# Kernel optimization log

Hardware: AMD Instinct MI355X
Metric: run time of the kernel (lower is better)

Reference implementation:

```python
import jax, jax.numpy as jnp
import numpy as np

DIM, E, H, HS = 2048, 8, 1408, 2816
B, S = 4, 2048


def setup_inputs() -> dict:
    key = jax.random.key(0)
    ks = jax.random.split(key, 12)
    sc = 0.02
    return {
        "x": jax.random.normal(ks[0], (B, S, DIM), jnp.float32),
        "gate_w": jax.random.normal(ks[1], (E, DIM), jnp.float32) * sc,
        "gate_b": jnp.zeros((E,), jnp.float32),
        "w1": jax.random.normal(ks[2], (E, H, DIM), jnp.float32) * sc,
        "b1": jnp.zeros((E, H), jnp.float32),
        "w3": jax.random.normal(ks[3], (E, H, DIM), jnp.float32) * sc,
        "b3": jnp.zeros((E, H), jnp.float32),
        "w2": jax.random.normal(ks[4], (E, DIM, H), jnp.float32) * sc,
        "b2": jnp.zeros((E, DIM), jnp.float32),
        "sh_gate": jax.random.normal(ks[5], (HS, DIM), jnp.float32) * sc,
        "sh_up": jax.random.normal(ks[6], (HS, DIM), jnp.float32) * sc,
        "sh_down": jax.random.normal(ks[7], (DIM, HS), jnp.float32) * sc,
        "top_k": 2,
    }


def reference(x, gate_w, gate_b, w1, b1, w3, b3, w2, b2, sh_gate, sh_up, sh_down, top_k):
    shape = x.shape
    xt = x.reshape(-1, DIM)                       # [T, D]
    T = xt.shape[0]

    # Router: softmax -> top-k (bias is None so gathered weights == topk probs)
    logits = xt @ gate_w.T + gate_b               # [T, E]
    scores = jax.nn.softmax(logits, axis=-1)
    topk_w, topk_idx = jax.lax.top_k(scores, top_k)  # [T, K]
    # combine weights per (token, expert); topk indices are distinct per row
    combine = jnp.zeros((T, E), xt.dtype).at[jnp.arange(T)[:, None], topk_idx].add(topk_w)

    # Routed experts: dense batched SwiGLU over all experts, weighted combine.
    g = jax.nn.silu(jnp.einsum("td,ehd->teh", xt, w1) + b1)  # [T, E, H]
    u = jnp.einsum("td,ehd->teh", xt, w3) + b3               # [T, E, H]
    hw = (g * u) * combine[:, :, None]                        # weight before down-proj
    routed = jnp.einsum("teh,edh->td", hw, w2) + combine @ b2  # [T, D]

    # Shared expert (bias-free SwiGLU)
    shared = (jax.nn.silu(xt @ sh_gate.T) * (xt @ sh_up.T)) @ sh_down.T

    return (shared + routed).reshape(shape)
```

## Files before the change

### kernel.cpp

```cpp
#include <hip/hip_runtime.h>
#include <stdint.h>

#define DIM  2048
#define NEXP 8
#define NH   1408
#define NHS  2816
#define NT   8192
#define NA   (NT*2)

typedef unsigned short u16;
typedef short bf16x8 __attribute__((ext_vector_type(8)));
typedef float f32x4 __attribute__((ext_vector_type(4)));

typedef __attribute__((address_space(1))) const uint32_t gas_u32;
typedef __attribute__((address_space(3))) uint32_t las_u32;

__device__ __forceinline__ u16 f2bf(float f) {
  uint32_t x = __builtin_bit_cast(uint32_t, f);
  x += 0x7FFFu + ((x >> 16) & 1u);
  return (u16)(x >> 16);
}

__device__ __forceinline__ void gload_lds16(const void* g, void* l) {
  __builtin_amdgcn_global_load_lds((gas_u32*)g, (las_u32*)l, 16, 0, 0);
}

__device__ __forceinline__ bool xcd_map_band(int G, int& nt, int& mt) {
  const int gx = gridDim.x;
  int f = blockIdx.y * gx + blockIdx.x;
  int xcd = f & 7;
  int local = f >> 3;
  if (G <= 0) return false;
  int band = (G + 7) >> 3;
  int slot = local % band;
  int ntv  = local / band;
  if (ntv >= gx) return false;
  int mtv = xcd * band + slot;
  if (mtv >= G) return false;
  nt = ntv; mt = mtv;
  return true;
}

struct alignas(16) US8 { u16 u[8]; };
struct alignas(8)  US4 { u16 u[4]; };

__global__ __launch_bounds__(256) void convert_kernel(const float* __restrict__ src,
                                                      u16* __restrict__ dst, int n8) {
  int i = blockIdx.x * 256 + threadIdx.x;
  if (i >= n8) return;
  const float4* s = (const float4*)src + (size_t)i * 2;
  float4 a = s[0], b = s[1];
  US8 r;
  r.u[0]=f2bf(a.x); r.u[1]=f2bf(a.y); r.u[2]=f2bf(a.z); r.u[3]=f2bf(a.w);
  r.u[4]=f2bf(b.x); r.u[5]=f2bf(b.y); r.u[6]=f2bf(b.z); r.u[7]=f2bf(b.w);
  *((US8*)dst + i) = r;
}

__global__ void zero_counts(int* counts) { if (threadIdx.x < NEXP) counts[threadIdx.x] = 0; }

__global__ __launch_bounds__(64) void router_kernel(const float* __restrict__ x,
    const float* __restrict__ gw, const float* __restrict__ gb,
    u16* __restrict__ xb,
    int* __restrict__ tope, float* __restrict__ topw, int* __restrict__ counts) {
  const int t = blockIdx.x;
  const int lane = threadIdx.x;
  const float4* xr = (const float4*)(x + (size_t)t * DIM);
  float4 xv[8];
  #pragma unroll
  for (int j = 0; j < 8; j++) xv[j] = xr[j * 64 + lane];
  US4* xrow = (US4*)(xb + (size_t)t * DIM);
  #pragma unroll
  for (int j = 0; j < 8; j++) {
    US4 r4;
    r4.u[0] = f2bf(xv[j].x); r4.u[1] = f2bf(xv[j].y);
    r4.u[2] = f2bf(xv[j].z); r4.u[3] = f2bf(xv[j].w);
    xrow[j * 64 + lane] = r4;
  }
  float p[NEXP];
  #pragma unroll
  for (int e = 0; e < NEXP; e++) {
    const float4* gr = (const float4*)(gw + (size_t)e * DIM);
    float s = 0.f;
    #pragma unroll
    for (int j = 0; j < 8; j++) {
      float4 g = gr[j * 64 + lane];
      s += xv[j].x*g.x + xv[j].y*g.y + xv[j].z*g.z + xv[j].w*g.w;
    }
    p[e] = s;
  }
  #pragma unroll
  for (int off = 32; off > 0; off >>= 1) {
    #pragma unroll
    for (int e = 0; e < NEXP; e++) p[e] += __shfl_xor(p[e], off);
  }
  if (lane == 0) {
    float pr[NEXP];
    float mx = -1e30f;
    #pragma unroll
    for (int e = 0; e < NEXP; e++) { p[e] += gb[e]; mx = fmaxf(mx, p[e]); }
    float den = 0.f;
    #pragma unroll
    for (int e = 0; e < NEXP; e++) { pr[e] = __expf(p[e] - mx); den += pr[e]; }
    float inv = 1.f / den;
    #pragma unroll
    for (int e = 0; e < NEXP; e++) pr[e] *= inv;
    int e0 = 0;
    #pragma unroll
    for (int e = 1; e < NEXP; e++) if (pr[e] > pr[e0]) e0 = e;
    int e1 = (e0 == 0) ? 1 : 0;
    #pragma unroll
    for (int e = 0; e < NEXP; e++) { if (e != e0 && pr[e] > pr[e1]) e1 = e; }
    tope[t*2]   = e0; tope[t*2+1] = e1;
    topw[t*2]   = pr[e0]; topw[t*2+1] = pr[e1];
    atomicAdd(&counts[e0], 1); atomicAdd(&counts[e1], 1);
  }
}

__global__ void scan_kernel(const int* __restrict__ counts, int* __restrict__ offsets,
                            int* __restrict__ cursor) {
  if (threadIdx.x == 0) {
    int s = 0;
    for (int e = 0; e < NEXP; e++) { offsets[e] = s; cursor[e] = s; s += counts[e]; }
    offsets[NEXP] = s;
  }
}

__global__ __launch_bounds__(256) void assign_kernel(const int* __restrict__ tope,
    const float* __restrict__ topw, int* __restrict__ cursor,
    int* __restrict__ ptok, float* __restrict__ pw) {
  int t = blockIdx.x * 256 + threadIdx.x;
  if (t >= NT) return;
  #pragma unroll
  for (int k = 0; k < 2; k++) {
    int e = tope[t*2+k];
    int pos = atomicAdd(&cursor[e], 1);
    ptok[pos] = t;
    pw[pos]   = topw[t*2+k];
  }
}

template<bool ROUTED>
__global__ __launch_bounds__(256, 2) void gemm_up(
    const u16* __restrict__ X, const u16* __restrict__ Wg, const u16* __restrict__ Wu,
    const float* __restrict__ Bg, const float* __restrict__ Bu,
    u16* __restrict__ Hout,
    const int* __restrict__ offsets, const int* __restrict__ ptok,
    const float* __restrict__ pw, int Nfeat)
{
  int e = 0, seg = 0, cnt = NT;
  if (ROUTED) {
    e = blockIdx.z;
    seg = offsets[e];
    cnt = offsets[e+1] - seg;
  }
  const int G = ROUTED ? ((cnt + 127) >> 7) : (int)gridDim.y;
  int nt, mt;
  if (!xcd_map_band(G, nt, mt)) return;
  const int m0 = mt * 128;
  const int tid = threadIdx.x;
  const int wave = tid >> 6, lane = tid & 63;

  __shared__ u16 sA[128*64];
  __shared__ u16 sBg[64*64];
  __shared__ u16 sBu[64*64];
  char* sAc  = (char*)sA;
  char* sBgc = (char*)sBg;
  char* sBuc = (char*)sBu;

  const u16* aSrc[4];
  #pragma unroll
  for (int j = 0; j < 4; j++) {
    int c = j * 256 + tid;
    int row = c >> 3, gch = (c & 7) ^ (row & 7);
    int r = m0 + row;
    size_t srow;
    if (ROUTED) { r = (r < cnt) ? r : (cnt - 1); srow = (size_t)ptok[seg + r]; }
    else        { srow = (size_t)r; }
    aSrc[j] = X + srow * DIM + gch * 8;
  }
  const size_t wOff = ROUTED ? (size_t)e * Nfeat * DIM : 0;
  const u16 *bgSrc[2], *buSrc[2];
  #pragma unroll
  for (int j = 0; j < 2; j++) {
    int c = j * 256 + tid;
    int row = c >> 3, gch = (c & 7) ^ (row & 7);
    bgSrc[j] = Wg + wOff + (size_t)(nt * 64 + row) * DIM + gch * 8;
    buSrc[j] = Wu + wOff + (size_t)(nt * 64 + row) * DIM + gch * 8;
  }

  f32x4 accg[4][2], accu[4][2];
  #pragma unroll
  for (int m = 0; m < 4; m++)
    #pragma unroll
    for (int n = 0; n < 2; n++) { accg[m][n] = (f32x4){0,0,0,0}; accu[m][n] = (f32x4){0,0,0,0}; }

  const int wr = (wave >> 1) * 64;
  const int wc = (wave & 1) * 32;
  const int lr = lane & 15, kg = lane >> 4;
  int aOff[4], bOff[2];
  #pragma unroll
  for (int m = 0; m < 4; m++) { int row = wr + m*16 + lr; aOff[m] = row*128 + ((kg ^ (row & 7)) & 7) * 16; }
  #pragma unroll
  for (int n = 0; n < 2; n++) { int row = wc + n*16 + lr; bOff[n] = row*128 + ((kg ^ (row & 7)) & 7) * 16; }

  for (int k0 = 0; k0 < DIM; k0 += 64) {
    __syncthreads();
    #pragma unroll
    for (int j = 0; j < 4; j++) gload_lds16(aSrc[j] + k0, sAc + j*4096 + wave*1024);
    #pragma unroll
    for (int j = 0; j < 2; j++) {
      gload_lds16(bgSrc[j] + k0, sBgc + j*4096 + wave*1024);
      gload_lds16(buSrc[j] + k0, sBuc + j*4096 + wave*1024);
    }
    __syncthreads();
    bf16x8 af[4][2], bgf[2][2], buf2[2][2];
    #pragma unroll
    for (int m = 0; m < 4; m++) {
      af[m][0] = *(const bf16x8*)(sAc + aOff[m]);
      af[m][1] = *(const bf16x8*)(sAc + (aOff[m] ^ 64));
    }
    #pragma unroll
    for (int n = 0; n < 2; n++) {
      bgf[n][0]  = *(const bf16x8*)(sBgc + bOff[n]);
      bgf[n][1]  = *(const bf16x8*)(sBgc + (bOff[n] ^ 64));
      buf2[n][0] = *(const bf16x8*)(sBuc + bOff[n]);
      buf2[n][1] = *(const bf16x8*)(sBuc + (bOff[n] ^ 64));
    }
    #pragma unroll
    for (int kk = 0; kk < 2; kk++)
      #pragma unroll
      for (int m = 0; m < 4; m++)
        #pragma unroll
        for (int n = 0; n < 2; n++) {
          accg[m][n] = __builtin_amdgcn_mfma_f32_16x16x32_bf16(af[m][kk], bgf[n][kk],  accg[m][n], 0, 0, 0);
          accu[m][n] = __builtin_amdgcn_mfma_f32_16x16x32_bf16(af[m][kk], buf2[n][kk], accu[m][n], 0, 0, 0);
        }
  }

  const int col0 = nt * 64 + wc;
  #pragma unroll
  for (int m = 0; m < 4; m++) {
    #pragma unroll
    for (int n = 0; n < 2; n++) {
      #pragma unroll
      for (int i = 0; i < 4; i++) {
        int rl = wr + m*16 + (lane >> 4) * 4 + i;
        int gr = m0 + rl;
        if (ROUTED && gr >= cnt) continue;
        int col = col0 + n*16 + (lane & 15);
        float g = accg[m][n][i];
        float u = accu[m][n][i];
        float scale = 1.f;
        size_t orow;
        if (ROUTED) {
          int ai = seg + gr;
          scale = pw[ai];
          g += Bg[e * Nfeat + col];
          u += Bu[e * Nfeat + col];
          orow = (size_t)ai;
        } else {
          orow = (size_t)gr;
        }
        float s = g / (1.f + __expf(-g));
        Hout[orow * (size_t)Nfeat + col] = f2bf(s * u * scale);
      }
    }
  }
}

template<bool ROUTED>
__global__ __launch_bounds__(256, 2) void gemm_down(
    const u16* __restrict__ Hin, const u16* __restrict__ W,
    const float* __restrict__ B2, float* __restrict__ Out,
    const int* __restrict__ offsets, const int* __restrict__ ptok,
    const float* __restrict__ pw, int Kdim)
{
  int e = 0, seg = 0, cnt = NT;
  if (ROUTED) {
    e = blockIdx.z;
    seg = offsets[e];
    cnt = offsets[e+1] - seg;
  }
  const int G = ROUTED ? ((cnt + 127) >> 7) : (int)gridDim.y;
  int nt, mt;
  if (!xcd_map_band(G, nt, mt)) return;
  const int m0 = mt * 128;
  const int tid = threadIdx.x;
  const int wave = tid >> 6, lane = tid & 63;

  __shared__ u16 sA[128*64];
  __shared__ u16 sB[128*64];
  char* sAc = (char*)sA;
  char* sBc = (char*)sB;

  const u16* aSrc[4]; const u16* bSrc[4];
  #pragma unroll
  for (int j = 0; j < 4; j++) {
    int c = j * 256 + tid;
    int row = c >> 3, gch = (c & 7) ^ (row & 7);
    int r = m0 + row;
    size_t arow;
    if (ROUTED) { r = (r < cnt) ? r : (cnt - 1); arow = (size_t)(seg + r); }
    else        { arow = (size_t)r; }
    aSrc[j] = Hin + arow * (size_t)Kdim + gch * 8;
    size_t brow = (size_t)(ROUTED ? e * DIM : 0) + nt * 128 + row;
    bSrc[j] = W + brow * (size_t)Kdim + gch * 8;
  }

  f32x4 acc[4][4];
  #pragma unroll
  for (int m = 0; m < 4; m++)
    #pragma unroll
    for (int n = 0; n < 4; n++) acc[m][n] = (f32x4){0,0,0,0};

  const int wr = (wave >> 1) * 64, wc = (wave & 1) * 64;
  const int lr = lane & 15, kg = lane >> 4;
  int aOff[4], bOff[4];
  #pragma unroll
  for (int m = 0; m < 4; m++) { int row = wr + m*16 + lr; aOff[m] = row*128 + ((kg ^ (row & 7)) & 7) * 16; }
  #pragma unroll
  for (int n = 0; n < 4; n++) { int row = wc + n*16 + lr; bOff[n] = row*128 + ((kg ^ (row & 7)) & 7) * 16; }

  for (int k0 = 0; k0 < Kdim; k0 += 64) {
    __syncthreads();
    #pragma unroll
    for (int j = 0; j < 4; j++) {
      gload_lds16(aSrc[j] + k0, sAc + j*4096 + wave*1024);
      gload_lds16(bSrc[j] + k0, sBc + j*4096 + wave*1024);
    }
    __syncthreads();
    bf16x8 af[4][2], bf[4][2];
    #pragma unroll
    for (int m = 0; m < 4; m++) {
      af[m][0] = *(const bf16x8*)(sAc + aOff[m]);
      af[m][1] = *(const bf16x8*)(sAc + (aOff[m] ^ 64));
    }
    #pragma unroll
    for (int n = 0; n < 4; n++) {
      bf[n][0] = *(const bf16x8*)(sBc + bOff[n]);
      bf[n][1] = *(const bf16x8*)(sBc + (bOff[n] ^ 64));
    }
    #pragma unroll
    for (int kk = 0; kk < 2; kk++)
      #pragma unroll
      for (int m = 0; m < 4; m++)
        #pragma unroll
        for (int n = 0; n < 4; n++)
          acc[m][n] = __builtin_amdgcn_mfma_f32_16x16x32_bf16(af[m][kk], bf[n][kk], acc[m][n], 0, 0, 0);
  }

  const int col0 = nt * 128 + wc;
  #pragma unroll
  for (int m = 0; m < 4; m++) {
    #pragma unroll
    for (int n = 0; n < 4; n++) {
      #pragma unroll
      for (int i = 0; i < 4; i++) {
        int rl = wr + m*16 + (lane >> 4) * 4 + i;
        int gr = m0 + rl;
        int col = col0 + n*16 + (lane & 15);
        float v = acc[m][n][i];
        if (ROUTED) {
          if (gr < cnt) {
            int ai = seg + gr;
            int token = ptok[ai];
            float w = pw[ai];
            atomicAdd(Out + (size_t)token * DIM + col, v + w * B2[e * DIM + col]);
          }
        } else {
          Out[(size_t)gr * DIM + col] = v;
        }
      }
    }
  }
}

extern "C" void kernel_launch(void* const* d_in, const int* in_sizes, int n_in,
                              void* d_out, int out_size, void* d_ws, size_t ws_size,
                              hipStream_t stream) {
  (void)in_sizes; (void)n_in; (void)out_size; (void)ws_size;
  const float* x      = (const float*)d_in[0];
  const float* gate_w = (const float*)d_in[1];
  const float* gate_b = (const float*)d_in[2];
  const float* w1     = (const float*)d_in[3];
  const float* b1     = (const float*)d_in[4];
  const float* w3     = (const float*)d_in[5];
  const float* b3     = (const float*)d_in[6];
  const float* w2     = (const float*)d_in[7];
  const float* b2     = (const float*)d_in[8];
  const float* shg    = (const float*)d_in[9];
  const float* shu    = (const float*)d_in[10];
  const float* shd    = (const float*)d_in[11];
  float* out = (float*)d_out;

  char* ws = (char*)d_ws;
  size_t off = 0;
  auto alloc = [&](size_t bytes) -> void* {
    void* p = ws + off;
    off += (bytes + 255) & ~(size_t)255;
    return p;
  };
  u16* xb    = (u16*)alloc((size_t)NT * DIM * 2);
  u16* w1b   = (u16*)alloc((size_t)NEXP * NH * DIM * 2);
  u16* w3b   = (u16*)alloc((size_t)NEXP * NH * DIM * 2);
  u16* w2b   = (u16*)alloc((size_t)NEXP * DIM * NH * 2);
  u16* shgb  = (u16*)alloc((size_t)NHS * DIM * 2);
  u16* shub  = (u16*)alloc((size_t)NHS * DIM * 2);
  u16* shdb  = (u16*)alloc((size_t)DIM * NHS * 2);
  u16* hsh   = (u16*)alloc((size_t)NT * NHS * 2);
  u16* hr    = (u16*)alloc((size_t)NA * NH * 2);
  int*   tope    = (int*)alloc(NT * 2 * 4);
  float* topw    = (float*)alloc(NT * 2 * 4);
  int*   ptok    = (int*)alloc(NA * 4);
  float* pw      = (float*)alloc(NA * 4);
  int*   counts  = (int*)alloc(64);
  int*   offsets = (int*)alloc(64);
  int*   cursor  = (int*)alloc(64);

  auto cvt = [&](const float* s, u16* d, size_t n) {
    int n8 = (int)(n / 8);
    convert_kernel<<<(n8 + 255) / 256, 256, 0, stream>>>(s, d, n8);
  };
  cvt(w1,  w1b,  (size_t)NEXP * NH * DIM);
  cvt(w3,  w3b,  (size_t)NEXP * NH * DIM);
  cvt(w2,  w2b,  (size_t)NEXP * DIM * NH);
  cvt(shg, shgb, (size_t)NHS * DIM);
  cvt(shu, shub, (size_t)NHS * DIM);
  cvt(shd, shdb, (size_t)DIM * NHS);

  zero_counts<<<1, 64, 0, stream>>>(counts);
  router_kernel<<<NT, 64, 0, stream>>>(x, gate_w, gate_b, xb, tope, topw, counts);
  scan_kernel<<<1, 1, 0, stream>>>(counts, offsets, cursor);
  assign_kernel<<<NT / 256, 256, 0, stream>>>(tope, topw, cursor, ptok, pw);

  gemm_up<false><<<dim3(NHS / 64, NT / 128, 1), 256, 0, stream>>>(
      xb, shgb, shub, nullptr, nullptr, hsh, nullptr, nullptr, nullptr, NHS);
  gemm_up<true><<<dim3(NH / 64, NT / 128, NEXP), 256, 0, stream>>>(
      xb, w1b, w3b, b1, b3, hr, offsets, ptok, pw, NH);
  gemm_down<false><<<dim3(DIM / 128, NT / 128, 1), 256, 0, stream>>>(
      hsh, shdb, nullptr, out, nullptr, nullptr, nullptr, NHS);
  gemm_down<true><<<dim3(DIM / 128, NT / 128, NEXP), 256, 0, stream>>>(
      hr, w2b, b2, out, offsets, ptok, pw, NH);
}
```

Before: 1.112 ms.

## Merge shared and routed GEMMs into single launches and fuse conversions

Combines the six weight-conversion kernels, the counter zeroing and an output zero-fill into one launch. The shared and routed expert up-projections now run in one grid that uses blockIdx.z to pick the expert, and the down-projections are merged the same way. Because the shared down-projection now runs concurrently with the routed blocks, it must accumulate with atomics into an output that is zeroed up front. This removes launch gaps and lets the wave tails of the shared and routed GEMMs overlap. The cost is extra atomic traffic on the shared output, the added zero-fill, and idle blocks in the routed z-slices of the up grid, which is sized to the wider shared layer.

```diff
diff --git a/kernel.cpp b/kernel.cpp
--- a/kernel.cpp
+++ b/kernel.cpp
@@ -25,16 +25,15 @@
   __builtin_amdgcn_global_load_lds((gas_u32*)g, (las_u32*)l, 16, 0, 0);
 }
 
-__device__ __forceinline__ bool xcd_map_band(int G, int& nt, int& mt) {
-  const int gx = gridDim.x;
-  int f = blockIdx.y * gx + blockIdx.x;
+__device__ __forceinline__ bool xcd_map_band(int gxa, int G, int& nt, int& mt) {
+  int f = blockIdx.y * gxa + blockIdx.x;
   int xcd = f & 7;
   int local = f >> 3;
   if (G <= 0) return false;
   int band = (G + 7) >> 3;
   int slot = local % band;
   int ntv  = local / band;
-  if (ntv >= gx) return false;
+  if (ntv >= gxa) return false;
   int mtv = xcd * band + slot;
   if (mtv >= G) return false;
   nt = ntv; mt = mtv;
@@ -44,19 +43,42 @@
 struct alignas(16) US8 { u16 u[8]; };
 struct alignas(8)  US4 { u16 u[4]; };
 
-__global__ __launch_bounds__(256) void convert_kernel(const float* __restrict__ src,
-                                                      u16* __restrict__ dst, int n8) {
+#define NB8 2883584
+#define NS8 720896
+#define NZ8 2097152
+#define CVT_TOTAL (3*NB8 + 3*NS8 + NZ8)
+
+__global__ __launch_bounds__(256) void convert_all(
+    const float* __restrict__ s0, const float* __restrict__ s1, const float* __restrict__ s2,
+    const float* __restrict__ s3, const float* __restrict__ s4, const float* __restrict__ s5,
+    u16* __restrict__ d0, u16* __restrict__ d1, u16* __restrict__ d2,
+    u16* __restrict__ d3, u16* __restrict__ d4, u16* __restrict__ d5,
+    float* __restrict__ outz, int* __restrict__ counts) {
+  if (blockIdx.x == 0 && threadIdx.x < NEXP) counts[threadIdx.x] = 0;
   int i = blockIdx.x * 256 + threadIdx.x;
-  if (i >= n8) return;
-  const float4* s = (const float4*)src + (size_t)i * 2;
-  float4 a = s[0], b = s[1];
+  if (i >= CVT_TOTAL) return;
+  if (i >= 3*NB8 + 3*NS8) {
+    int j = i - (3*NB8 + 3*NS8);
+    float4 z = {0.f, 0.f, 0.f, 0.f};
+    ((float4*)outz)[j*2]   = z;
+    ((float4*)outz)[j*2+1] = z;
+    return;
+  }
+  const float* s; u16* d; int base;
+  if      (i < NB8)            { s = s0; d = d0; base = 0; }
+  else if (i < 2*NB8)          { s = s1; d = d1; base = NB8; }
+  else if (i < 3*NB8)          { s = s2; d = d2; base = 2*NB8; }
+  else if (i < 3*NB8 + NS8)    { s = s3; d = d3; base = 3*NB8; }
+  else if (i < 3*NB8 + 2*NS8)  { s = s4; d = d4; base = 3*NB8 + NS8; }
+  else                         { s = s5; d = d5; base = 3*NB8 + 2*NS8; }
+  int j = i - base;
+  const float4* sp = (const float4*)s + (size_t)j * 2;
+  float4 a = sp[0], b = sp[1];
   US8 r;
   r.u[0]=f2bf(a.x); r.u[1]=f2bf(a.y); r.u[2]=f2bf(a.z); r.u[3]=f2bf(a.w);
   r.u[4]=f2bf(b.x); r.u[5]=f2bf(b.y); r.u[6]=f2bf(b.z); r.u[7]=f2bf(b.w);
-  *((US8*)dst + i) = r;
-}
-
-__global__ void zero_counts(int* counts) { if (threadIdx.x < NEXP) counts[threadIdx.x] = 0; }
+  *((US8*)d + j) = r;
+}
 
 __global__ __launch_bounds__(64) void router_kernel(const float* __restrict__ x,
     const float* __restrict__ gw, const float* __restrict__ gb,
@@ -139,23 +161,32 @@
   }
 }
 
-template<bool ROUTED>
-__global__ __launch_bounds__(256, 2) void gemm_up(
-    const u16* __restrict__ X, const u16* __restrict__ Wg, const u16* __restrict__ Wu,
-    const float* __restrict__ Bg, const float* __restrict__ Bu,
-    u16* __restrict__ Hout,
+__global__ __launch_bounds__(256, 2) void gemm_up_all(
+    const u16* __restrict__ X,
+    const u16* __restrict__ WgSh, const u16* __restrict__ WuSh, u16* __restrict__ HSh,
+    const u16* __restrict__ WgRt, const u16* __restrict__ WuRt,
+    const float* __restrict__ Bg, const float* __restrict__ Bu, u16* __restrict__ HRt,
     const int* __restrict__ offsets, const int* __restrict__ ptok,
-    const float* __restrict__ pw, int Nfeat)
+    const float* __restrict__ pw)
 {
-  int e = 0, seg = 0, cnt = NT;
-  if (ROUTED) {
-    e = blockIdx.z;
+  const int z = blockIdx.z;
+  const bool routed = (z > 0);
+  int e = 0, seg = 0, cnt = NT, Nfeat = NHS, gxa = NHS / 64;
+  const u16* Wg = WgSh; const u16* Wu = WuSh;
+  u16* Hout = HSh;
+  if (routed) {
+    e = z - 1;
     seg = offsets[e];
     cnt = offsets[e+1] - seg;
-  }
-  const int G = ROUTED ? ((cnt + 127) >> 7) : (int)gridDim.y;
+    Nfeat = NH; gxa = NH / 64;
+    if ((int)blockIdx.x >= gxa) return;
+    Wg = WgRt + (size_t)e * NH * DIM;
+    Wu = WuRt + (size_t)e * NH * DIM;
+    Hout = HRt;
+  }
+  const int G = routed ? ((cnt + 127) >> 7) : (NT / 128);
   int nt, mt;
-  if (!xcd_map_band(G, nt, mt)) return;
+  if (!xcd_map_band(gxa, G, nt, mt)) return;
   const int m0 = mt * 128;
   const int tid = threadIdx.x;
   const int wave = tid >> 6, lane = tid & 63;
@@ -174,18 +205,17 @@
     int row = c >> 3, gch = (c & 7) ^ (row & 7);
     int r = m0 + row;
     size_t srow;
-    if (ROUTED) { r = (r < cnt) ? r : (cnt - 1); srow = (size_t)ptok[seg + r]; }
+    if (routed) { r = (r < cnt) ? r : (cnt - 1); srow = (size_t)ptok[seg + r]; }
     else        { srow = (size_t)r; }
     aSrc[j] = X + srow * DIM + gch * 8;
   }
-  const size_t wOff = ROUTED ? (size_t)e * Nfeat * DIM : 0;
   const u16 *bgSrc[2], *buSrc[2];
   #pragma unroll
   for (int j = 0; j < 2; j++) {
     int c = j * 256 + tid;
     int row = c >> 3, gch = (c & 7) ^ (row & 7);
-    bgSrc[j] = Wg + wOff + (size_t)(nt * 64 + row) * DIM + gch * 8;
-    buSrc[j] = Wu + wOff + (size_t)(nt * 64 + row) * DIM + gch * 8;
+    bgSrc[j] = Wg + (size_t)(nt * 64 + row) * DIM + gch * 8;
+    buSrc[j] = Wu + (size_t)(nt * 64 + row) * DIM + gch * 8;
   }
 
   f32x4 accg[4][2], accu[4][2];
@@ -246,17 +276,17 @@
       for (int i = 0; i < 4; i++) {
         int rl = wr + m*16 + (lane >> 4) * 4 + i;
         int gr = m0 + rl;
-        if (ROUTED && gr >= cnt) continue;
+        if (routed && gr >= cnt) continue;
         int col = col0 + n*16 + (lane & 15);
         float g = accg[m][n][i];
         float u = accu[m][n][i];
         float scale = 1.f;
         size_t orow;
-        if (ROUTED) {
+        if (routed) {
           int ai = seg + gr;
           scale = pw[ai];
-          g += Bg[e * Nfeat + col];
-          u += Bu[e * Nfeat + col];
+          g += Bg[e * NH + col];
+          u += Bu[e * NH + col];
           orow = (size_t)ai;
         } else {
           orow = (size_t)gr;
@@ -268,22 +298,28 @@
   }
 }
 
-template<bool ROUTED>
-__global__ __launch_bounds__(256, 2) void gemm_down(
-    const u16* __restrict__ Hin, const u16* __restrict__ W,
+__global__ __launch_bounds__(256, 2) void gemm_down_all(
+    const u16* __restrict__ HSh, const u16* __restrict__ Wsh,
+    const u16* __restrict__ HRt, const u16* __restrict__ Wrt,
     const float* __restrict__ B2, float* __restrict__ Out,
     const int* __restrict__ offsets, const int* __restrict__ ptok,
-    const float* __restrict__ pw, int Kdim)
+    const float* __restrict__ pw)
 {
-  int e = 0, seg = 0, cnt = NT;
-  if (ROUTED) {
-    e = blockIdx.z;
+  const int z = blockIdx.z;
+  const bool routed = (z > 0);
+  int e = 0, seg = 0, cnt = NT, Kdim = NHS;
+  const u16* Hin = HSh; const u16* W = Wsh;
+  if (routed) {
+    e = z - 1;
     seg = offsets[e];
     cnt = offsets[e+1] - seg;
-  }
-  const int G = ROUTED ? ((cnt + 127) >> 7) : (int)gridDim.y;
+    Kdim = NH;
+    Hin = HRt;
+    W = Wrt + (size_t)e * DIM * NH;
+  }
+  const int G = routed ? ((cnt + 127) >> 7) : (NT / 128);
   int nt, mt;
-  if (!xcd_map_band(G, nt, mt)) return;
+  if (!xcd_map_band((int)gridDim.x, G, nt, mt)) return;
   const int m0 = mt * 128;
   const int tid = threadIdx.x;
   const int wave = tid >> 6, lane = tid & 63;
@@ -300,11 +336,10 @@
     int row = c >> 3, gch = (c & 7) ^ (row & 7);
     int r = m0 + row;
     size_t arow;
-    if (ROUTED) { r = (r < cnt) ? r : (cnt - 1); arow = (size_t)(seg + r); }
+    if (routed) { r = (r < cnt) ? r : (cnt - 1); arow = (size_t)(seg + r); }
     else        { arow = (size_t)r; }
     aSrc[j] = Hin + arow * (size_t)Kdim + gch * 8;
-    size_t brow = (size_t)(ROUTED ? e * DIM : 0) + nt * 128 + row;
-    bSrc[j] = W + brow * (size_t)Kdim + gch * 8;
+    bSrc[j] = W + (size_t)(nt * 128 + row) * Kdim + gch * 8;
   }
 
   f32x4 acc[4][4];
@@ -360,15 +395,14 @@
         int gr = m0 + rl;
         int col = col0 + n*16 + (lane & 15);
         float v = acc[m][n][i];
-        if (ROUTED) {
+        if (routed) {
           if (gr < cnt) {
             int ai = seg + gr;
             int token = ptok[ai];
-            float w = pw[ai];
-            atomicAdd(Out + (size_t)token * DIM + col, v + w * B2[e * DIM + col]);
+            atomicAdd(Out + (size_t)token * DIM + col, v + pw[ai] * B2[e * DIM + col]);
           }
         } else {
-          Out[(size_t)gr * DIM + col] = v;
+          atomicAdd(Out + (size_t)gr * DIM + col, v);
         }
       }
     }
@@ -417,28 +451,15 @@
   int*   offsets = (int*)alloc(64);
   int*   cursor  = (int*)alloc(64);
 
-  auto cvt = [&](const float* s, u16* d, size_t n) {
-    int n8 = (int)(n / 8);
-    convert_kernel<<<(n8 + 255) / 256, 256, 0, stream>>>(s, d, n8);
-  };
-  cvt(w1,  w1b,  (size_t)NEXP * NH * DIM);
-  cvt(w3,  w3b,  (size_t)NEXP * NH * DIM);
-  cvt(w2,  w2b,  (size_t)NEXP * DIM * NH);
-  cvt(shg, shgb, (size_t)NHS * DIM);
-  cvt(shu, shub, (size_t)NHS * DIM);
-  cvt(shd, shdb, (size_t)DIM * NHS);
-
-  zero_counts<<<1, 64, 0, stream>>>(counts);
+  convert_all<<<(CVT_TOTAL + 255) / 256, 256, 0, stream>>>(
+      w1, w3, w2, shg, shu, shd,
+      w1b, w3b, w2b, shgb, shub, shdb,
+      out, counts);
   router_kernel<<<NT, 64, 0, stream>>>(x, gate_w, gate_b, xb, tope, topw, counts);
   scan_kernel<<<1, 1, 0, stream>>>(counts, offsets, cursor);
   assign_kernel<<<NT / 256, 256, 0, stream>>>(tope, topw, cursor, ptok, pw);
-
-  gemm_up<false><<<dim3(NHS / 64, NT / 128, 1), 256, 0, stream>>>(
-      xb, shgb, shub, nullptr, nullptr, hsh, nullptr, nullptr, nullptr, NHS);
-  gemm_up<true><<<dim3(NH / 64, NT / 128, NEXP), 256, 0, stream>>>(
-      xb, w1b, w3b, b1, b3, hr, offsets, ptok, pw, NH);
-  gemm_down<false><<<dim3(DIM / 128, NT / 128, 1), 256, 0, stream>>>(
-      hsh, shdb, nullptr, out, nullptr, nullptr, nullptr, NHS);
-  gemm_down<true><<<dim3(DIM / 128, NT / 128, NEXP), 256, 0, stream>>>(
-      hr, w2b, b2, out, offsets, ptok, pw, NH);
-}
+  gemm_up_all<<<dim3(NHS / 64, NT / 128, 1 + NEXP), 256, 0, stream>>>(
+      xb, shgb, shub, hsh, w1b, w3b, b1, b3, hr, offsets, ptok, pw);
+  gemm_down_all<<<dim3(DIM / 128, NT / 128, 1 + NEXP), 256, 0, stream>>>(
+      hsh, shdb, hr, w2b, b2, out, offsets, ptok, pw);
+}
```

Result: slower. 1.136 ms (+2.1%).
